# Kernel optimization log

Measured on AMD Instinct MI355X. Metric: run time of the kernel, lower is better.

The kernel has to match this reference:

```python
import jax, jax.numpy as jnp
import numpy as np

N, E, EMB, H, HD, T, NG = 2048, 65536, 256, 8, 32, 24, 8


def _linear_params(key, din, dout):
    k1, k2 = jax.random.split(key)
    s = 1.0 / np.sqrt(din)
    W = jax.random.uniform(k1, (din, dout), minval=-s, maxval=s, dtype=jnp.float32)
    b = jax.random.uniform(k2, (dout,), minval=-s, maxval=s, dtype=jnp.float32)
    return W, b


def setup_inputs() -> dict:
    key = jax.random.key(0)
    ks = jax.random.split(key, 16)
    x = jax.random.normal(ks[0], (N, EMB), dtype=jnp.float32)
    edge_index = jax.random.randint(ks[1], (2, E), 0, N, dtype=jnp.int64)
    edge_attr = jax.random.normal(ks[2], (E, 4), dtype=jnp.float32)
    batch = jnp.sort(jax.random.randint(ks[3], (N,), 0, NG, dtype=jnp.int64))
    time_index = jax.random.randint(ks[4], (N,), 0, T, dtype=jnp.int64)
    temporal_embeddings = jax.random.normal(ks[5], (T, EMB), dtype=jnp.float32)
    Wq, bq = _linear_params(ks[6], EMB, EMB)
    Wk, bk = _linear_params(ks[7], EMB, EMB)
    Wv, bv = _linear_params(ks[8], EMB, EMB)
    Wo, bo = _linear_params(ks[9], EMB, EMB)
    We, be = _linear_params(ks[10], 4, H)
    Wtq, btq = _linear_params(ks[11], EMB, EMB)
    Wtk, btk = _linear_params(ks[12], EMB, EMB)
    Wtv, btv = _linear_params(ks[13], EMB, EMB)
    return dict(x=x, edge_index=edge_index, edge_attr=edge_attr, batch=batch,
                time_index=time_index, temporal_embeddings=temporal_embeddings,
                Wq=Wq, bq=bq, Wk=Wk, bk=bk, Wv=Wv, bv=bv, Wo=Wo, bo=bo,
                We=We, be=be, Wtq=Wtq, btq=btq, Wtk=Wtk, btk=btk, Wtv=Wtv, btv=btv)


def _heads(X, n):
    # [n, EMB] -> [H, n, HD]
    return X.reshape(n, H, HD).transpose(1, 0, 2)


def reference(x, edge_index, edge_attr, batch, time_index, temporal_embeddings,
              Wq, bq, Wk, bk, Wv, bv, Wo, bo, We, be, Wtq, btq, Wtk, btk, Wtv, btv):
    n = x.shape[0]
    scale = HD ** -0.5

    Qh = _heads(x @ Wq + bq, n)
    Kh = _heads(x @ Wk + bk, n)
    Vh = _heads(x @ Wv + bv, n)
    scores = jnp.einsum('hnd,hmd->hnm', Qh, Kh) * scale  # [H, n, n]

    # edge bias: vectorized scatter-add of per-edge per-head biases into [H, n, n]
    src, dst = edge_index[0], edge_index[1]
    valid = (src >= 0) & (src < n) & (dst >= 0) & (dst < n)
    eb = edge_attr @ We + be                              # [E, H]
    eb = jnp.where(valid[:, None], eb, 0.0)
    srcc = jnp.clip(src, 0, n - 1)
    dstc = jnp.clip(dst, 0, n - 1)
    scores = scores.at[:, srcc, dstc].add(eb.T)

    # batch mask: nodes may only attend within their own graph
    same_graph = batch[:, None] == batch[None, :]          # [n, n]
    scores = jnp.where(same_graph[None, :, :], scores, -jnp.inf)

    attn = jax.nn.softmax(scores, axis=-1)
    spatial_out = jnp.einsum('hnm,hmd->hnd', attn, Vh)     # [H, n, HD]

    # temporal attention on gathered temporal embeddings
    ti = jnp.clip(time_index, 0, temporal_embeddings.shape[0] - 1)
    emb = temporal_embeddings[ti]                          # [n, EMB]
    TQ = _heads(emb @ Wtq + btq, n)
    TK = _heads(emb @ Wtk + btk, n)
    TV = _heads(emb @ Wtv + btv, n)
    t_scores = jnp.einsum('hnd,hmd->hnm', TQ, TK) * scale
    t_scores = jnp.where(same_graph[None, :, :], t_scores, -jnp.inf)
    t_attn = jax.nn.softmax(t_scores, axis=-1)
    temporal_out = jnp.einsum('hnm,hmd->hnd', t_attn, TV)

    combined = (spatial_out + temporal_out).transpose(1, 0, 2).reshape(n, EMB)
    return combined @ Wo + bo
```

## Files before the change

### kernel.cpp

```cpp
#include <hip/hip_runtime.h>
#include <cstdint>
#include <cstddef>

#define EMB 256
#define NH 8
#define HD 32
#define NG 8
#define TMAX 24

#define LMAX 384
#define LB 384
#define TPB 12
#define VRU 200
#define FM 8.0f

typedef short s16x8 __attribute__((ext_vector_type(8)));
typedef float f32x4 __attribute__((ext_vector_type(4)));

__device__ __forceinline__ unsigned short f2b(float f) {
    unsigned u = __float_as_uint(f);
    return (unsigned short)((u + 0x7FFFu + ((u >> 16) & 1u)) >> 16);
}
__device__ __forceinline__ float b2f(unsigned short h) {
    return __uint_as_float((unsigned)h << 16);
}
__device__ __forceinline__ unsigned long long pack4(unsigned short a, unsigned short b,
                                                    unsigned short c, unsigned short d) {
    return (unsigned long long)a | ((unsigned long long)b << 16) |
           ((unsigned long long)c << 32) | ((unsigned long long)d << 48);
}

__device__ __forceinline__ size_t afrag_idx(int row, int k) {
    return ((size_t)((row >> 4) * 8 + (k >> 5)) << 9) +
           ((((k >> 3) & 3) * 16 + (row & 15)) << 3) + (k & 7);
}

struct PrepArgs {
    float4* Bias4; int bias4;
    const float* x; unsigned short* xh; unsigned short* xl;
    const float* temb; const int* ti; unsigned short* eh; unsigned short* el;
    const float* W[7]; unsigned short* whb; unsigned short* wlb;
    const int* batch; int* gstart; int n;
    int zb, cvtb;
};

__global__ __launch_bounds__(256) void k_prep(PrepArgs pa) {
    __shared__ float tile[32][33];
    int b = blockIdx.x;
    const int t = threadIdx.x;

    if (b < pa.zb) {
        int i = b * 256 + t;
        if (i < pa.bias4) pa.Bias4[i] = make_float4(0.f, 0.f, 0.f, 0.f);
        return;
    }
    b -= pa.zb;
    if (b < pa.cvtb) {
        int i = b * 256 + t;
        if (i < pa.n * (EMB / 4)) {
            int row = i >> 6, k4 = (i & 63) * 4;
            float4 v = ((const float4*)pa.x)[i];
            unsigned short h0 = f2b(v.x), h1 = f2b(v.y), h2 = f2b(v.z), h3 = f2b(v.w);
            size_t o = afrag_idx(row, k4) >> 2;
            ((unsigned long long*)pa.xh)[o] = pack4(h0, h1, h2, h3);
            ((unsigned long long*)pa.xl)[o] = pack4(f2b(v.x - b2f(h0)), f2b(v.y - b2f(h1)),
                                                    f2b(v.z - b2f(h2)), f2b(v.w - b2f(h3)));
        }
        return;
    }
    b -= pa.cvtb;
    if (b < pa.cvtb) {
        int idx = b * 256 + t;
        if (idx < pa.n * (EMB / 4)) {
            int row = idx >> 6, k4 = (idx & 63) * 4;
            int tt = pa.ti[row];
            tt = tt < 0 ? 0 : (tt > TMAX - 1 ? TMAX - 1 : tt);
            float4 v = ((const float4*)pa.temb)[tt * (EMB / 4) + (idx & 63)];
            unsigned short h0 = f2b(v.x), h1 = f2b(v.y), h2 = f2b(v.z), h3 = f2b(v.w);
            size_t o = afrag_idx(row, k4) >> 2;
            ((unsigned long long*)pa.eh)[o] = pack4(h0, h1, h2, h3);
            ((unsigned long long*)pa.el)[o] = pack4(f2b(v.x - b2f(h0)), f2b(v.y - b2f(h1)),
                                                    f2b(v.z - b2f(h2)), f2b(v.w - b2f(h3)));
        }
        return;
    }
    b -= pa.cvtb;
    if (b < 448) {
        const int z = b >> 6, rem = b & 63;
        const int k0 = (rem >> 3) << 5, n0 = (rem & 7) << 5;
        const float* W = pa.W[z];
        unsigned short* Wh = pa.whb + (size_t)z * 65536;
        unsigned short* Wl = pa.wlb + (size_t)z * 65536;
        {
            int rr = t >> 3, c4 = (t & 7) * 4;
            float4 v = *(const float4*)(W + (size_t)(k0 + rr) * 256 + n0 + c4);
            tile[rr][c4 + 0] = v.x; tile[rr][c4 + 1] = v.y;
            tile[rr][c4 + 2] = v.z; tile[rr][c4 + 3] = v.w;
        }
        __syncthreads();
        {
            int nn = n0 + (t >> 3), k4 = (t & 7) * 4;
            float v0 = tile[k4 + 0][t >> 3], v1 = tile[k4 + 1][t >> 3];
            float v2 = tile[k4 + 2][t >> 3], v3 = tile[k4 + 3][t >> 3];
            unsigned short h0 = f2b(v0), h1 = f2b(v1), h2 = f2b(v2), h3 = f2b(v3);
            size_t o = afrag_idx(nn, k0 + k4) >> 2;
            ((unsigned long long*)Wh)[o] = pack4(h0, h1, h2, h3);
            ((unsigned long long*)Wl)[o] = pack4(f2b(v0 - b2f(h0)), f2b(v1 - b2f(h1)),
                                                 f2b(v2 - b2f(h2)), f2b(v3 - b2f(h3)));
        }
        return;
    }
    if (t <= NG) {
        int lo = 0, hi = pa.n;
        while (lo < hi) {
            int mid = (lo + hi) >> 1;
            if (pa.batch[mid] < t) lo = mid + 1; else hi = mid;
        }
        pa.gstart[t] = lo;
    }
}

struct GB {
    const unsigned short* Ah[6];
    const unsigned short* Al[6];
    const float* bias[6];
    unsigned short* Chi[6];
    unsigned short* Clo[6];
    float cscale[6];
};

__global__ __launch_bounds__(256) void k_gemm_split(GB gb,
        const unsigned short* __restrict__ whb, const unsigned short* __restrict__ wlb, int M,
        const int* __restrict__ ei, const float* __restrict__ eattr,
        const float* __restrict__ We, const float* __restrict__ be,
        const int* __restrict__ batch, const int* __restrict__ gstart,
        float* __restrict__ Bias, int E) {
    const int z = blockIdx.z;
    const int t = threadIdx.x;

    if (z == 6) {
        const int stride = gridDim.x * gridDim.y * 256;
        for (int e = (blockIdx.y * gridDim.x + blockIdx.x) * 256 + t; e < E; e += stride) {
            int src = ei[e], dst = ei[E + e];
            if (src < 0 || src >= M || dst < 0 || dst >= M) continue;
            int bs = batch[src];
            if (bs != batch[dst]) continue;
            float4 a = *(const float4*)(eattr + (size_t)e * 4);
            int col = dst - gstart[bs];
#pragma unroll
            for (int h = 0; h < NH; h++) {
                float v = a.x * We[0 * NH + h] + a.y * We[1 * NH + h] +
                          a.z * We[2 * NH + h] + a.w * We[3 * NH + h] + be[h];
                atomicAdd(Bias + ((size_t)h * M + src) * LB + col, v);
            }
        }
        return;
    }

    const unsigned short* Ah = gb.Ah[z];
    const unsigned short* Al = gb.Al[z];
    const unsigned short* Wh = whb + (size_t)z * 65536;
    const unsigned short* Wl = wlb + (size_t)z * 65536;
    const float* bias = gb.bias[z];
    unsigned short* Chi = gb.Chi[z];
    unsigned short* Clo = gb.Clo[z];
    const float cs = gb.cscale[z];

    const int lane = t & 63, wv = t >> 6, lr = lane & 15, lq = lane >> 4;
    const int bm = blockIdx.x * 64 + (wv >> 1) * 32;
    const int bn = blockIdx.y * 64 + (wv & 1) * 32;
    const int mg0 = bm >> 4, ng0 = bn >> 4;

    f32x4 acc[2][2] = {};
#pragma unroll
    for (int kc = 0; kc < 8; kc++) {
        s16x8 ah[2], al[2], bh[2], bl[2];
#pragma unroll
        for (int mi = 0; mi < 2; mi++) {
            size_t o = ((size_t)((mg0 + mi) * 8 + kc) << 9) + lane * 8;
            ah[mi] = *(const s16x8*)(Ah + o);
            al[mi] = *(const s16x8*)(Al + o);
        }
#pragma unroll
        for (int ni = 0; ni < 2; ni++) {
            size_t o = ((size_t)((ng0 + ni) * 8 + kc) << 9) + lane * 8;
            bh[ni] = *(const s16x8*)(Wh + o);
            bl[ni] = *(const s16x8*)(Wl + o);
        }
#pragma unroll
        for (int mi = 0; mi < 2; mi++)
#pragma unroll
            for (int ni = 0; ni < 2; ni++) {
                acc[mi][ni] = __builtin_amdgcn_mfma_f32_16x16x32_bf16(al[mi], bh[ni], acc[mi][ni], 0, 0, 0);
                acc[mi][ni] = __builtin_amdgcn_mfma_f32_16x16x32_bf16(ah[mi], bl[ni], acc[mi][ni], 0, 0, 0);
                acc[mi][ni] = __builtin_amdgcn_mfma_f32_16x16x32_bf16(ah[mi], bh[ni], acc[mi][ni], 0, 0, 0);
            }
    }
#pragma unroll
    for (int ni = 0; ni < 2; ni++) {
        const int col = bn + ni * 16 + lr;
        const int hh = col >> 5, dd = col & 31;
        float bv = bias[col];
#pragma unroll
        for (int mi = 0; mi < 2; mi++) {
#pragma unroll
            for (int r = 0; r < 4; r++) {
                int crow = bm + mi * 16 + 4 * lq + r;
                if (crow < M) {
                    float val = (acc[mi][ni][r] + bv) * cs;
                    unsigned short h = f2b(val);
                    size_t o = ((size_t)hh * M + crow) * HD + dd;
                    Chi[o] = h;
                    if (Clo) Clo[o] = f2b(val - b2f(h));
                }
            }
        }
    }
}

__global__ __launch_bounds__(128) void k_attn4(
    const unsigned short* __restrict__ Qh, const unsigned short* __restrict__ Ql,
    const unsigned short* __restrict__ K, const unsigned short* __restrict__ V,
    const unsigned short* __restrict__ TQh, const unsigned short* __restrict__ TQl,
    const unsigned short* __restrict__ TK, const unsigned short* __restrict__ TV,
    const int* __restrict__ gstart, const float* __restrict__ Bias,
    float* __restrict__ s_out, float* __restrict__ t_out, int n) {

    const int g  = blockIdx.x / TPB;
    const int tp = blockIdx.x % TPB;
    const int h  = blockIdx.y;
    const int tz = blockIdx.z;
    const int gs = gstart[g], ge = gstart[g + 1];
    const int L  = ge - gs;
    const int q0b = tp * 32;
    if (q0b >= L) return;
    const int NC = (L + 31) >> 5;

    const unsigned short* Qph = tz ? TQh : Qh;
    const unsigned short* Qpl = tz ? TQl : Ql;
    const unsigned short* Kp  = tz ? TK  : K;
    const unsigned short* Vp  = tz ? TV  : V;
    float* outp = tz ? t_out : s_out;
    const bool hasb = (tz == 0);

    __shared__ __align__(16) unsigned int Vt[32 * VRU];
    __shared__ __align__(16) unsigned short Pb[2][16][40];

    const int t = threadIdx.x;
    const int wv = t >> 6, lane = t & 63;
    const int lr = lane & 15, lq = lane >> 4;
    const size_t hb = (size_t)h * n;

    {
        const int d0 = (t & 7) * 4;
        for (int jp = t >> 3; jp < NC * 16; jp += 16) {
            int j0 = jp * 2;
            unsigned short a0 = 0, a1 = 0, a2 = 0, a3 = 0, b0 = 0, b1 = 0, b2 = 0, b3 = 0;
            if (j0 < L) {
                const unsigned short* vp = Vp + (hb + gs + j0) * HD + d0;
                a0 = vp[0]; a1 = vp[1]; a2 = vp[2]; a3 = vp[3];
            }
            if (j0 + 1 < L) {
                const unsigned short* vp = Vp + (hb + gs + j0 + 1) * HD + d0;
                b0 = vp[0]; b1 = vp[1]; b2 = vp[2]; b3 = vp[3];
            }
            Vt[(d0 + 0) * VRU + jp] = (unsigned)a0 | ((unsigned)b0 << 16);
            Vt[(d0 + 1) * VRU + jp] = (unsigned)a1 | ((unsigned)b1 << 16);
            Vt[(d0 + 2) * VRU + jp] = (unsigned)a2 | ((unsigned)b2 << 16);
            Vt[(d0 + 3) * VRU + jp] = (unsigned)a3 | ((unsigned)b3 << 16);
        }
    }

    const int q0w = q0b + wv * 16;
    int gq = gs + q0w + lr;
    if (gq > ge - 1) gq = ge - 1;
    s16x8 qfh = *(const s16x8*)(Qph + (hb + gq) * HD + lq * 8);
    s16x8 qfl = *(const s16x8*)(Qpl + (hb + gq) * HD + lq * 8);
    __syncthreads();
    if (q0w >= L) return;

    const float* br0 = Bias; const float* br1 = Bias;
    const float* br2 = Bias; const float* br3 = Bias;
    if (hasb) {
        int r0 = gs + q0w + 4 * lq;
        int a0 = r0 + 0 < n ? r0 + 0 : n - 1;
        int a1 = r0 + 1 < n ? r0 + 1 : n - 1;
        int a2 = r0 + 2 < n ? r0 + 2 : n - 1;
        int a3 = r0 + 3 < n ? r0 + 3 : n - 1;
        br0 = Bias + (hb + a0) * LB;
        br1 = Bias + (hb + a1) * LB;
        br2 = Bias + (hb + a2) * LB;
        br3 = Bias + (hb + a3) * LB;
    }

    auto loadK = [&](int c, int half) -> s16x8 {
        int key = (2 * c + half) * 16 + lr;
        int krow = (key < L) ? (gs + key) : (ge - 1);
        return *(const s16x8*)(Kp + (hb + krow) * HD + lq * 8);
    };

    f32x4 acc0 = {0.f, 0.f, 0.f, 0.f};
    f32x4 acc1 = {0.f, 0.f, 0.f, 0.f};
    float ps0 = 0.f, ps1 = 0.f, ps2 = 0.f, ps3 = 0.f;

    s16x8 kfa = loadK(0, 0), kfb = loadK(0, 1);
    for (int c = 0; c < NC; c++) {
        const int cn = (c + 1 < NC) ? c + 1 : c;
        s16x8 nka = loadK(cn, 0), nkb = loadK(cn, 1);

        float p[2][4];
#pragma unroll
        for (int half = 0; half < 2; half++) {
            const int key = (2 * c + half) * 16 + lr;
            s16x8 kf = half ? kfb : kfa;
            f32x4 d = {0.f, 0.f, 0.f, 0.f};
            d = __builtin_amdgcn_mfma_f32_16x16x32_bf16(qfl, kf, d, 0, 0, 0);
            d = __builtin_amdgcn_mfma_f32_16x16x32_bf16(qfh, kf, d, 0, 0, 0);
            float s0 = d[0], s1 = d[1], s2 = d[2], s3 = d[3];
            if (hasb) {
                s0 += br0[key]; s1 += br1[key]; s2 += br2[key]; s3 += br3[key];
            }
            const bool ok = key < L;
            s0 = ok ? s0 : -3.0e38f;
            s1 = ok ? s1 : -3.0e38f;
            s2 = ok ? s2 : -3.0e38f;
            s3 = ok ? s3 : -3.0e38f;
            p[half][0] = __expf(s0 - FM);
            p[half][1] = __expf(s1 - FM);
            p[half][2] = __expf(s2 - FM);
            p[half][3] = __expf(s3 - FM);
        }
        ps0 += p[0][0] + p[1][0];
        ps1 += p[0][1] + p[1][1];
        ps2 += p[0][2] + p[1][2];
        ps3 += p[0][3] + p[1][3];
#pragma unroll
        for (int half = 0; half < 2; half++) {
#pragma unroll
            for (int r = 0; r < 4; r++)
                Pb[wv][4 * lq + r][half * 16 + lr] = f2b(p[half][r]);
        }
        s16x8 pf  = *(const s16x8*)&Pb[wv][lr][8 * lq];
        s16x8 vf0 = *(const s16x8*)&Vt[(size_t)lr * VRU + c * 16 + lq * 4];
        s16x8 vf1 = *(const s16x8*)&Vt[(size_t)(16 + lr) * VRU + c * 16 + lq * 4];
        acc0 = __builtin_amdgcn_mfma_f32_16x16x32_bf16(pf, vf0, acc0, 0, 0, 0);
        acc1 = __builtin_amdgcn_mfma_f32_16x16x32_bf16(pf, vf1, acc1, 0, 0, 0);
        kfa = nka; kfb = nkb;
    }

#pragma unroll
    for (int m = 1; m < 16; m <<= 1) {
        ps0 += __shfl_xor(ps0, m, 16);
        ps1 += __shfl_xor(ps1, m, 16);
        ps2 += __shfl_xor(ps2, m, 16);
        ps3 += __shfl_xor(ps3, m, 16);
    }
    float iv0 = 1.0f / ps0, iv1 = 1.0f / ps1, iv2 = 1.0f / ps2, iv3 = 1.0f / ps3;
    const int qb = q0w + 4 * lq;
#pragma unroll
    for (int r = 0; r < 4; r++) {
        float iv = r == 0 ? iv0 : (r == 1 ? iv1 : (r == 2 ? iv2 : iv3));
        if (qb + r < L) {
            float* op = outp + (hb + gs + qb + r) * HD + lr;
            op[0]  = acc0[r] * iv;
            op[16] = acc1[r] * iv;
        }
    }
}

__global__ __launch_bounds__(256) void k_gemm_out(const float* __restrict__ A1,
        const float* __restrict__ A2,
        const unsigned short* __restrict__ Wh, const unsigned short* __restrict__ Wl,
        const float* __restrict__ bias, float* __restrict__ C, int M) {
    const int t = threadIdx.x;
    const int lane = t & 63, wv = t >> 6, lr = lane & 15, lq = lane >> 4;
    const int bm = blockIdx.x * 64 + (wv >> 1) * 32;
    const int bn = blockIdx.y * 64 + (wv & 1) * 32;
    const int ng0 = bn >> 4;

    int ra[2], cb[2];
#pragma unroll
    for (int mi = 0; mi < 2; mi++) {
        int r = bm + mi * 16 + lr;
        ra[mi] = r < M ? r : M - 1;
    }
#pragma unroll
    for (int ni = 0; ni < 2; ni++) cb[ni] = bn + ni * 16 + lr;

    f32x4 acc[2][2] = {};
#pragma unroll
    for (int kc = 0; kc < 8; kc++) {
        s16x8 ah[2], al[2], bh[2], bl[2];
#pragma unroll
        for (int mi = 0; mi < 2; mi++) {
            size_t off = ((size_t)kc * M + ra[mi]) * HD + lq * 8;
            float4 a = *(const float4*)(A1 + off);
            float4 b = *(const float4*)(A1 + off + 4);
            float4 c2 = *(const float4*)(A2 + off);
            float4 d2 = *(const float4*)(A2 + off + 4);
            float vv[8] = {a.x + c2.x, a.y + c2.y, a.z + c2.z, a.w + c2.w,
                           b.x + d2.x, b.y + d2.y, b.z + d2.z, b.w + d2.w};
#pragma unroll
            for (int j = 0; j < 8; j++) {
                unsigned short hh = f2b(vv[j]);
                ah[mi][j] = (short)hh;
                al[mi][j] = (short)f2b(vv[j] - b2f(hh));
            }
        }
#pragma unroll
        for (int ni = 0; ni < 2; ni++) {
            size_t o = ((size_t)((ng0 + ni) * 8 + kc) << 9) + lane * 8;
            bh[ni] = *(const s16x8*)(Wh + o);
            bl[ni] = *(const s16x8*)(Wl + o);
        }
#pragma unroll
        for (int mi = 0; mi < 2; mi++)
#pragma unroll
            for (int ni = 0; ni < 2; ni++) {
                acc[mi][ni] = __builtin_amdgcn_mfma_f32_16x16x32_bf16(al[mi], bh[ni], acc[mi][ni], 0, 0, 0);
                acc[mi][ni] = __builtin_amdgcn_mfma_f32_16x16x32_bf16(ah[mi], bl[ni], acc[mi][ni], 0, 0, 0);
                acc[mi][ni] = __builtin_amdgcn_mfma_f32_16x16x32_bf16(ah[mi], bh[ni], acc[mi][ni], 0, 0, 0);
            }
    }
#pragma unroll
    for (int ni = 0; ni < 2; ni++) {
        float bv = bias[cb[ni]];
#pragma unroll
        for (int mi = 0; mi < 2; mi++) {
#pragma unroll
            for (int r = 0; r < 4; r++) {
                int crow = bm + mi * 16 + 4 * lq + r;
                if (crow < M)
                    C[(size_t)crow * 256 + cb[ni]] = acc[mi][ni][r] + bv;
            }
        }
    }
}

extern "C" void kernel_launch(void* const* d_in, const int* in_sizes, int n_in,
                              void* d_out, int out_size, void* d_ws, size_t ws_size,
                              hipStream_t stream) {
    const float* x     = (const float*)d_in[0];
    const int*   ei    = (const int*)d_in[1];
    const float* eattr = (const float*)d_in[2];
    const int*   batch = (const int*)d_in[3];
    const int*   ti    = (const int*)d_in[4];
    const float* temb  = (const float*)d_in[5];
    const float* Wq = (const float*)d_in[6],  *bq = (const float*)d_in[7];
    const float* Wk = (const float*)d_in[8],  *bk = (const float*)d_in[9];
    const float* Wv = (const float*)d_in[10], *bv = (const float*)d_in[11];
    const float* Wo = (const float*)d_in[12], *bo = (const float*)d_in[13];
    const float* We = (const float*)d_in[14], *be = (const float*)d_in[15];
    const float* Wtq = (const float*)d_in[16], *btq = (const float*)d_in[17];
    const float* Wtk = (const float*)d_in[18], *btk = (const float*)d_in[19];
    const float* Wtv = (const float*)d_in[20], *btv = (const float*)d_in[21];

    const int n = in_sizes[0] / EMB;
    const int E = in_sizes[2] / 4;
    float* out = (float*)d_out;

    char* w = (char*)d_ws;
    auto alloc = [&](size_t bytes) -> void* {
        void* p = (void*)w;
        w += (bytes + 255) & ~(size_t)255;
        return p;
    };
    const size_t nb = (size_t)n * EMB * 2;
    unsigned short* xh   = (unsigned short*)alloc(nb);
    unsigned short* xl   = (unsigned short*)alloc(nb);
    unsigned short* eh   = (unsigned short*)alloc(nb);
    unsigned short* el   = (unsigned short*)alloc(nb);
    unsigned short* whb  = (unsigned short*)alloc((size_t)7 * 65536 * 2);
    unsigned short* wlb  = (unsigned short*)alloc((size_t)7 * 65536 * 2);
    unsigned short* Qhb  = (unsigned short*)alloc(nb);
    unsigned short* Qlb  = (unsigned short*)alloc(nb);
    unsigned short* Kb   = (unsigned short*)alloc(nb);
    unsigned short* Vb   = (unsigned short*)alloc(nb);
    unsigned short* TQhb = (unsigned short*)alloc(nb);
    unsigned short* TQlb = (unsigned short*)alloc(nb);
    unsigned short* TKb  = (unsigned short*)alloc(nb);
    unsigned short* TVb  = (unsigned short*)alloc(nb);
    float* Bias  = (float*)alloc((size_t)NH * n * LB * 4);
    float* s_out = (float*)alloc((size_t)n * EMB * 4);
    float* t_out = (float*)alloc((size_t)n * EMB * 4);
    int* gstart  = (int*)alloc((NG + 1) * 4);

    PrepArgs pa;
    pa.Bias4 = (float4*)Bias;
    pa.bias4 = NH * n * LB / 4;
    pa.x = x; pa.xh = xh; pa.xl = xl;
    pa.temb = temb; pa.ti = ti; pa.eh = eh; pa.el = el;
    pa.W[0] = Wq; pa.W[1] = Wk; pa.W[2] = Wv;
    pa.W[3] = Wtq; pa.W[4] = Wtk; pa.W[5] = Wtv; pa.W[6] = Wo;
    pa.whb = whb; pa.wlb = wlb;
    pa.batch = batch; pa.gstart = gstart; pa.n = n;
    pa.zb = (pa.bias4 + 255) / 256;
    pa.cvtb = (n * (EMB / 4) + 255) / 256;
    const int prep_blocks = pa.zb + 2 * pa.cvtb + 448 + 1;
    k_prep<<<dim3(prep_blocks), dim3(256), 0, stream>>>(pa);

    const float scale = 0.17677669529663687f;
    GB gb;
    gb.Ah[0] = xh; gb.Al[0] = xl; gb.bias[0] = bq;  gb.Chi[0] = Qhb;  gb.Clo[0] = Qlb;  gb.cscale[0] = scale;
    gb.Ah[1] = xh; gb.Al[1] = xl; gb.bias[1] = bk;  gb.Chi[1] = Kb;   gb.Clo[1] = nullptr; gb.cscale[1] = 1.f;
    gb.Ah[2] = xh; gb.Al[2] = xl; gb.bias[2] = bv;  gb.Chi[2] = Vb;   gb.Clo[2] = nullptr; gb.cscale[2] = 1.f;
    gb.Ah[3] = eh; gb.Al[3] = el; gb.bias[3] = btq; gb.Chi[3] = TQhb; gb.Clo[3] = TQlb; gb.cscale[3] = scale;
    gb.Ah[4] = eh; gb.Al[4] = el; gb.bias[4] = btk; gb.Chi[4] = TKb;  gb.Clo[4] = nullptr; gb.cscale[4] = 1.f;
    gb.Ah[5] = eh; gb.Al[5] = el; gb.bias[5] = btv; gb.Chi[5] = TVb;  gb.Clo[5] = nullptr; gb.cscale[5] = 1.f;
    k_gemm_split<<<dim3((n + 63) / 64, EMB / 64, 7), dim3(256), 0, stream>>>(
        gb, whb, wlb, n, ei, eattr, We, be, batch, gstart, Bias, E);

    k_attn4<<<dim3(NG * TPB, NH, 2), dim3(128), 0, stream>>>(Qhb, Qlb, Kb, Vb,
                                                             TQhb, TQlb, TKb, TVb,
                                                             gstart, Bias, s_out, t_out, n);
    k_gemm_out<<<dim3((n + 63) / 64, EMB / 64), dim3(256), 0, stream>>>(
        s_out, t_out, whb + (size_t)6 * 65536, wlb + (size_t)6 * 65536, bo, out, n);
}
```

Baseline: 68.02 us.

## Fuse spatial and temporal attention into one block and sum outputs in-kernel

```diff
diff --git a/kernel.cpp b/kernel.cpp
--- a/kernel.cpp
+++ b/kernel.cpp
@@ -10,7 +10,7 @@
 
 #define LMAX 384
 #define LB 384
-#define TPB 12
+#define TPB 6
 #define VRU 200
 #define FM 8.0f
 
@@ -218,158 +218,166 @@
     }
 }
 
-__global__ __launch_bounds__(128) void k_attn4(
+__global__ __launch_bounds__(256) void k_attn5(
     const unsigned short* __restrict__ Qh, const unsigned short* __restrict__ Ql,
     const unsigned short* __restrict__ K, const unsigned short* __restrict__ V,
     const unsigned short* __restrict__ TQh, const unsigned short* __restrict__ TQl,
     const unsigned short* __restrict__ TK, const unsigned short* __restrict__ TV,
     const int* __restrict__ gstart, const float* __restrict__ Bias,
-    float* __restrict__ s_out, float* __restrict__ t_out, int n) {
+    float* __restrict__ comb, int n) {
 
     const int g  = blockIdx.x / TPB;
     const int tp = blockIdx.x % TPB;
     const int h  = blockIdx.y;
-    const int tz = blockIdx.z;
     const int gs = gstart[g], ge = gstart[g + 1];
     const int L  = ge - gs;
-    const int q0b = tp * 32;
+    const int q0b = tp * 64;
     if (q0b >= L) return;
     const int NC = (L + 31) >> 5;
 
-    const unsigned short* Qph = tz ? TQh : Qh;
-    const unsigned short* Qpl = tz ? TQl : Ql;
-    const unsigned short* Kp  = tz ? TK  : K;
-    const unsigned short* Vp  = tz ? TV  : V;
-    float* outp = tz ? t_out : s_out;
-    const bool hasb = (tz == 0);
-
     __shared__ __align__(16) unsigned int Vt[32 * VRU];
-    __shared__ __align__(16) unsigned short Pb[2][16][40];
+    __shared__ __align__(16) unsigned short Pb[4][16][40];
 
     const int t = threadIdx.x;
     const int wv = t >> 6, lane = t & 63;
     const int lr = lane & 15, lq = lane >> 4;
     const size_t hb = (size_t)h * n;
 
-    {
-        const int d0 = (t & 7) * 4;
-        for (int jp = t >> 3; jp < NC * 16; jp += 16) {
-            int j0 = jp * 2;
-            unsigned short a0 = 0, a1 = 0, a2 = 0, a3 = 0, b0 = 0, b1 = 0, b2 = 0, b3 = 0;
-            if (j0 < L) {
-                const unsigned short* vp = Vp + (hb + gs + j0) * HD + d0;
-                a0 = vp[0]; a1 = vp[1]; a2 = vp[2]; a3 = vp[3];
-            }
-            if (j0 + 1 < L) {
-                const unsigned short* vp = Vp + (hb + gs + j0 + 1) * HD + d0;
-                b0 = vp[0]; b1 = vp[1]; b2 = vp[2]; b3 = vp[3];
-            }
-            Vt[(d0 + 0) * VRU + jp] = (unsigned)a0 | ((unsigned)b0 << 16);
-            Vt[(d0 + 1) * VRU + jp] = (unsigned)a1 | ((unsigned)b1 << 16);
-            Vt[(d0 + 2) * VRU + jp] = (unsigned)a2 | ((unsigned)b2 << 16);
-            Vt[(d0 + 3) * VRU + jp] = (unsigned)a3 | ((unsigned)b3 << 16);
-        }
-    }
-
     const int q0w = q0b + wv * 16;
     int gq = gs + q0w + lr;
     if (gq > ge - 1) gq = ge - 1;
-    s16x8 qfh = *(const s16x8*)(Qph + (hb + gq) * HD + lq * 8);
-    s16x8 qfl = *(const s16x8*)(Qpl + (hb + gq) * HD + lq * 8);
-    __syncthreads();
-    if (q0w >= L) return;
-
-    const float* br0 = Bias; const float* br1 = Bias;
-    const float* br2 = Bias; const float* br3 = Bias;
-    if (hasb) {
-        int r0 = gs + q0w + 4 * lq;
-        int a0 = r0 + 0 < n ? r0 + 0 : n - 1;
-        int a1 = r0 + 1 < n ? r0 + 1 : n - 1;
-        int a2 = r0 + 2 < n ? r0 + 2 : n - 1;
-        int a3 = r0 + 3 < n ? r0 + 3 : n - 1;
-        br0 = Bias + (hb + a0) * LB;
-        br1 = Bias + (hb + a1) * LB;
-        br2 = Bias + (hb + a2) * LB;
-        br3 = Bias + (hb + a3) * LB;
-    }
-
-    auto loadK = [&](int c, int half) -> s16x8 {
-        int key = (2 * c + half) * 16 + lr;
-        int krow = (key < L) ? (gs + key) : (ge - 1);
-        return *(const s16x8*)(Kp + (hb + krow) * HD + lq * 8);
-    };
-
-    f32x4 acc0 = {0.f, 0.f, 0.f, 0.f};
-    f32x4 acc1 = {0.f, 0.f, 0.f, 0.f};
-    float ps0 = 0.f, ps1 = 0.f, ps2 = 0.f, ps3 = 0.f;
-
-    s16x8 kfa = loadK(0, 0), kfb = loadK(0, 1);
-    for (int c = 0; c < NC; c++) {
-        const int cn = (c + 1 < NC) ? c + 1 : c;
-        s16x8 nka = loadK(cn, 0), nkb = loadK(cn, 1);
-
-        float p[2][4];
-#pragma unroll
-        for (int half = 0; half < 2; half++) {
-            const int key = (2 * c + half) * 16 + lr;
-            s16x8 kf = half ? kfb : kfa;
-            f32x4 d = {0.f, 0.f, 0.f, 0.f};
-            d = __builtin_amdgcn_mfma_f32_16x16x32_bf16(qfl, kf, d, 0, 0, 0);
-            d = __builtin_amdgcn_mfma_f32_16x16x32_bf16(qfh, kf, d, 0, 0, 0);
-            float s0 = d[0], s1 = d[1], s2 = d[2], s3 = d[3];
-            if (hasb) {
-                s0 += br0[key]; s1 += br1[key]; s2 += br2[key]; s3 += br3[key];
-            }
-            const bool ok = key < L;
-            s0 = ok ? s0 : -3.0e38f;
-            s1 = ok ? s1 : -3.0e38f;
-            s2 = ok ? s2 : -3.0e38f;
-            s3 = ok ? s3 : -3.0e38f;
-            p[half][0] = __expf(s0 - FM);
-            p[half][1] = __expf(s1 - FM);
-            p[half][2] = __expf(s2 - FM);
-            p[half][3] = __expf(s3 - FM);
-        }
-        ps0 += p[0][0] + p[1][0];
-        ps1 += p[0][1] + p[1][1];
-        ps2 += p[0][2] + p[1][2];
-        ps3 += p[0][3] + p[1][3];
-#pragma unroll
-        for (int half = 0; half < 2; half++) {
-#pragma unroll
-            for (int r = 0; r < 4; r++)
-                Pb[wv][4 * lq + r][half * 16 + lr] = f2b(p[half][r]);
-        }
-        s16x8 pf  = *(const s16x8*)&Pb[wv][lr][8 * lq];
-        s16x8 vf0 = *(const s16x8*)&Vt[(size_t)lr * VRU + c * 16 + lq * 4];
-        s16x8 vf1 = *(const s16x8*)&Vt[(size_t)(16 + lr) * VRU + c * 16 + lq * 4];
-        acc0 = __builtin_amdgcn_mfma_f32_16x16x32_bf16(pf, vf0, acc0, 0, 0, 0);
-        acc1 = __builtin_amdgcn_mfma_f32_16x16x32_bf16(pf, vf1, acc1, 0, 0, 0);
-        kfa = nka; kfb = nkb;
-    }
-
-#pragma unroll
-    for (int m = 1; m < 16; m <<= 1) {
-        ps0 += __shfl_xor(ps0, m, 16);
-        ps1 += __shfl_xor(ps1, m, 16);
-        ps2 += __shfl_xor(ps2, m, 16);
-        ps3 += __shfl_xor(ps3, m, 16);
-    }
-    float iv0 = 1.0f / ps0, iv1 = 1.0f / ps1, iv2 = 1.0f / ps2, iv3 = 1.0f / ps3;
+
+    float os0[4] = {0.f, 0.f, 0.f, 0.f};
+    float os1[4] = {0.f, 0.f, 0.f, 0.f};
+
+    for (int tz = 0; tz < 2; tz++) {
+        const unsigned short* Qph = tz ? TQh : Qh;
+        const unsigned short* Qpl = tz ? TQl : Ql;
+        const unsigned short* Kp  = tz ? TK  : K;
+        const unsigned short* Vp  = tz ? TV  : V;
+        const bool hasb = (tz == 0);
+
+        if (tz) __syncthreads();
+
+        {
+            const int d0 = (t & 7) * 4;
+            for (int jp = t >> 3; jp < NC * 16; jp += 32) {
+                int j0 = jp * 2;
+                unsigned short a0 = 0, a1 = 0, a2 = 0, a3 = 0, b0 = 0, b1 = 0, b2 = 0, b3 = 0;
+                if (j0 < L) {
+                    const unsigned short* vp = Vp + (hb + gs + j0) * HD + d0;
+                    a0 = vp[0]; a1 = vp[1]; a2 = vp[2]; a3 = vp[3];
+                }
+                if (j0 + 1 < L) {
+                    const unsigned short* vp = Vp + (hb + gs + j0 + 1) * HD + d0;
+                    b0 = vp[0]; b1 = vp[1]; b2 = vp[2]; b3 = vp[3];
+                }
+                Vt[(d0 + 0) * VRU + jp] = (unsigned)a0 | ((unsigned)b0 << 16);
+                Vt[(d0 + 1) * VRU + jp] = (unsigned)a1 | ((unsigned)b1 << 16);
+                Vt[(d0 + 2) * VRU + jp] = (unsigned)a2 | ((unsigned)b2 << 16);
+                Vt[(d0 + 3) * VRU + jp] = (unsigned)a3 | ((unsigned)b3 << 16);
+            }
+        }
+
+        s16x8 qfh = *(const s16x8*)(Qph + (hb + gq) * HD + lq * 8);
+        s16x8 qfl = *(const s16x8*)(Qpl + (hb + gq) * HD + lq * 8);
+        __syncthreads();
+
+        const float* br0 = Bias; const float* br1 = Bias;
+        const float* br2 = Bias; const float* br3 = Bias;
+        if (hasb) {
+            int r0 = gs + q0w + 4 * lq;
+            int a0 = r0 + 0 < n ? r0 + 0 : n - 1;
+            int a1 = r0 + 1 < n ? r0 + 1 : n - 1;
+            int a2 = r0 + 2 < n ? r0 + 2 : n - 1;
+            int a3 = r0 + 3 < n ? r0 + 3 : n - 1;
+            br0 = Bias + (hb + a0) * LB;
+            br1 = Bias + (hb + a1) * LB;
+            br2 = Bias + (hb + a2) * LB;
+            br3 = Bias + (hb + a3) * LB;
+        }
+
+        auto loadK = [&](int c, int half) -> s16x8 {
+            int key = (2 * c + half) * 16 + lr;
+            int krow = (key < L) ? (gs + key) : (ge - 1);
+            return *(const s16x8*)(Kp + (hb + krow) * HD + lq * 8);
+        };
+
+        f32x4 acc0 = {0.f, 0.f, 0.f, 0.f};
+        f32x4 acc1 = {0.f, 0.f, 0.f, 0.f};
+        float ps0 = 0.f, ps1 = 0.f, ps2 = 0.f, ps3 = 0.f;
+
+        s16x8 kfa = loadK(0, 0), kfb = loadK(0, 1);
+        for (int c = 0; c < NC; c++) {
+            const int cn = (c + 1 < NC) ? c + 1 : c;
+            s16x8 nka = loadK(cn, 0), nkb = loadK(cn, 1);
+
+            float p[2][4];
+#pragma unroll
+            for (int half = 0; half < 2; half++) {
+                const int key = (2 * c + half) * 16 + lr;
+                s16x8 kf = half ? kfb : kfa;
+                f32x4 d = {0.f, 0.f, 0.f, 0.f};
+                d = __builtin_amdgcn_mfma_f32_16x16x32_bf16(qfl, kf, d, 0, 0, 0);
+                d = __builtin_amdgcn_mfma_f32_16x16x32_bf16(qfh, kf, d, 0, 0, 0);
+                float s0 = d[0], s1 = d[1], s2 = d[2], s3 = d[3];
+                if (hasb) {
+                    s0 += br0[key]; s1 += br1[key]; s2 += br2[key]; s3 += br3[key];
+                }
+                const bool ok = key < L;
+                s0 = ok ? s0 : -3.0e38f;
+                s1 = ok ? s1 : -3.0e38f;
+                s2 = ok ? s2 : -3.0e38f;
+                s3 = ok ? s3 : -3.0e38f;
+                p[half][0] = __expf(s0 - FM);
+                p[half][1] = __expf(s1 - FM);
+                p[half][2] = __expf(s2 - FM);
+                p[half][3] = __expf(s3 - FM);
+            }
+            ps0 += p[0][0] + p[1][0];
+            ps1 += p[0][1] + p[1][1];
+            ps2 += p[0][2] + p[1][2];
+            ps3 += p[0][3] + p[1][3];
+#pragma unroll
+            for (int half = 0; half < 2; half++) {
+#pragma unroll
+                for (int r = 0; r < 4; r++)
+                    Pb[wv][4 * lq + r][half * 16 + lr] = f2b(p[half][r]);
+            }
+            s16x8 pf  = *(const s16x8*)&Pb[wv][lr][8 * lq];
+            s16x8 vf0 = *(const s16x8*)&Vt[(size_t)lr * VRU + c * 16 + lq * 4];
+            s16x8 vf1 = *(const s16x8*)&Vt[(size_t)(16 + lr) * VRU + c * 16 + lq * 4];
+            acc0 = __builtin_amdgcn_mfma_f32_16x16x32_bf16(pf, vf0, acc0, 0, 0, 0);
+            acc1 = __builtin_amdgcn_mfma_f32_16x16x32_bf16(pf, vf1, acc1, 0, 0, 0);
+            kfa = nka; kfb = nkb;
+        }
+
+#pragma unroll
+        for (int m = 1; m < 16; m <<= 1) {
+            ps0 += __shfl_xor(ps0, m, 16);
+            ps1 += __shfl_xor(ps1, m, 16);
+            ps2 += __shfl_xor(ps2, m, 16);
+            ps3 += __shfl_xor(ps3, m, 16);
+        }
+        float iv0 = 1.0f / ps0, iv1 = 1.0f / ps1, iv2 = 1.0f / ps2, iv3 = 1.0f / ps3;
+        os0[0] += acc0[0] * iv0; os1[0] += acc1[0] * iv0;
+        os0[1] += acc0[1] * iv1; os1[1] += acc1[1] * iv1;
+        os0[2] += acc0[2] * iv2; os1[2] += acc1[2] * iv2;
+        os0[3] += acc0[3] * iv3; os1[3] += acc1[3] * iv3;
+    }
+
     const int qb = q0w + 4 * lq;
 #pragma unroll
     for (int r = 0; r < 4; r++) {
-        float iv = r == 0 ? iv0 : (r == 1 ? iv1 : (r == 2 ? iv2 : iv3));
         if (qb + r < L) {
-            float* op = outp + (hb + gs + qb + r) * HD + lr;
-            op[0]  = acc0[r] * iv;
-            op[16] = acc1[r] * iv;
-        }
-    }
-}
-
-__global__ __launch_bounds__(256) void k_gemm_out(const float* __restrict__ A1,
-        const float* __restrict__ A2,
+            float* op = comb + (hb + gs + qb + r) * HD + lr;
+            op[0]  = os0[r];
+            op[16] = os1[r];
+        }
+    }
+}
+
+__global__ __launch_bounds__(256) void k_gemm_out(const float* __restrict__ A,
         const unsigned short* __restrict__ Wh, const unsigned short* __restrict__ Wl,
         const float* __restrict__ bias, float* __restrict__ C, int M) {
     const int t = threadIdx.x;
@@ -394,12 +402,9 @@
 #pragma unroll
         for (int mi = 0; mi < 2; mi++) {
             size_t off = ((size_t)kc * M + ra[mi]) * HD + lq * 8;
-            float4 a = *(const float4*)(A1 + off);
-            float4 b = *(const float4*)(A1 + off + 4);
-            float4 c2 = *(const float4*)(A2 + off);
-            float4 d2 = *(const float4*)(A2 + off + 4);
-            float vv[8] = {a.x + c2.x, a.y + c2.y, a.z + c2.z, a.w + c2.w,
-                           b.x + d2.x, b.y + d2.y, b.z + d2.z, b.w + d2.w};
+            float4 a = *(const float4*)(A + off);
+            float4 b = *(const float4*)(A + off + 4);
+            float vv[8] = {a.x, a.y, a.z, a.w, b.x, b.y, b.z, b.w};
 #pragma unroll
             for (int j = 0; j < 8; j++) {
                 unsigned short hh = f2b(vv[j]);
@@ -481,8 +486,7 @@
     unsigned short* TKb  = (unsigned short*)alloc(nb);
     unsigned short* TVb  = (unsigned short*)alloc(nb);
     float* Bias  = (float*)alloc((size_t)NH * n * LB * 4);
-    float* s_out = (float*)alloc((size_t)n * EMB * 4);
-    float* t_out = (float*)alloc((size_t)n * EMB * 4);
+    float* comb  = (float*)alloc((size_t)n * EMB * 4);
     int* gstart  = (int*)alloc((NG + 1) * 4);
 
     PrepArgs pa;
@@ -510,9 +514,9 @@
     k_gemm_split<<<dim3((n + 63) / 64, EMB / 64, 7), dim3(256), 0, stream>>>(
         gb, whb, wlb, n, ei, eattr, We, be, batch, gstart, Bias, E);
 
-    k_attn4<<<dim3(NG * TPB, NH, 2), dim3(128), 0, stream>>>(Qhb, Qlb, Kb, Vb,
-                                                             TQhb, TQlb, TKb, TVb,
-                                                             gstart, Bias, s_out, t_out, n);
+    k_attn5<<<dim3(NG * TPB, NH), dim3(256), 0, stream>>>(Qhb, Qlb, Kb, Vb,
+                                                          TQhb, TQlb, TKb, TVb,
+                                                          gstart, Bias, comb, n);
     k_gemm_out<<<dim3((n + 63) / 64, EMB / 64), dim3(256), 0, stream>>>(
-        s_out, t_out, whb + (size_t)6 * 65536, wlb + (size_t)6 * 65536, bo, out, n);
-}
+        comb, whb + (size_t)6 * 65536, wlb + (size_t)6 * 65536, bo, out, n);
+}
```

Result: faster. 62.37 us (-8.3%).
